# Kernel tuning notes

Hardware: AMD Instinct MI355X
Metric: run time of the kernel (lower is better)

The kernel has to match this reference:

```python
import jax, jax.numpy as jnp
import numpy as np

D_MODEL = 96
D_STATE = 16
D_INNER = 192   # expand * d_model
DT_RANK = 6     # ceil(96/16)
D_DEPTH_OUT = 1024  # (64/2)*(64/2)
BATCH, HH, WW = 2, 64, 64


def silu(v):
    return v * jax.nn.sigmoid(v)


def setup_inputs() -> dict:
    key = jax.random.key(0)
    ks = jax.random.split(key, 10)
    f = jnp.float32
    x = jax.random.normal(ks[0], (BATCH, HH, WW, D_MODEL), f)
    in_proj_w = jax.random.normal(ks[1], (2 * D_INNER, D_MODEL), f) * 0.02
    conv2d_w = jax.random.normal(ks[2], (D_INNER, 1, 3, 3), f) * 0.1  # depthwise, groups=D_INNER
    conv2d_b = jnp.zeros((D_INNER,), f)
    depth_conv_w = jax.random.normal(ks[3], (D_INNER, 1, 3, 3), f) * 0.1  # depthwise, stride 2
    depth_conv_b = jnp.zeros((D_INNER,), f)
    depth_fc_w = jax.random.normal(ks[4], (D_INNER, D_DEPTH_OUT), f) * 0.02
    depth_fc_b = jnp.zeros((D_INNER,), f)
    x_proj_w = jax.random.normal(ks[5], (DT_RANK + 2 * D_STATE, D_INNER), f) * 0.02
    dt_init_std = DT_RANK ** (-0.5)
    dt_projs_w = jax.random.uniform(ks[6], (D_INNER, DT_RANK), f, -dt_init_std, dt_init_std)
    # inverse-softplus of dt ~ U(log 1e-3, log 0.1)
    dt = jnp.exp(jax.random.uniform(ks[7], (D_INNER,), f) * (np.log(0.1) - np.log(0.001)) + np.log(0.001))
    dt = jnp.clip(dt, 1e-4, None)
    dt_projs_b = dt + jnp.log(-jnp.expm1(-dt))
    A_logs = jnp.log(jnp.tile(jnp.arange(1, D_STATE + 1, dtype=f)[None, :], (D_INNER, 1)))
    Ds = jnp.ones((D_INNER,), f)
    out_norm_w = jnp.ones((D_INNER,), f)
    out_norm_b = jnp.zeros((D_INNER,), f)
    out_proj_w = jax.random.normal(ks[8], (D_MODEL, D_INNER), f) * 0.02
    return dict(x=x, in_proj_w=in_proj_w, conv2d_w=conv2d_w, conv2d_b=conv2d_b,
                depth_conv_w=depth_conv_w, depth_conv_b=depth_conv_b,
                depth_fc_w=depth_fc_w, depth_fc_b=depth_fc_b, x_proj_w=x_proj_w,
                dt_projs_w=dt_projs_w, dt_projs_b=dt_projs_b, A_logs=A_logs, Ds=Ds,
                out_norm_w=out_norm_w, out_norm_b=out_norm_b, out_proj_w=out_proj_w)


def _selective_scan(u, delta, A, Bm, Cm, D, delta_bias):
    # u, delta: [B, D, L]; A: [D, N]; Bm, Cm: [B, N, L]; D: [D]; delta_bias: [D]
    delta = jax.nn.softplus(delta + delta_bias[None, :, None])
    dA = jnp.exp(jnp.einsum('bdl,dn->lbdn', delta, A))          # [L,B,D,N]
    dBu = jnp.einsum('bdl,bnl,bdl->lbdn', delta, Bm, u)          # [L,B,D,N]
    Ct = jnp.transpose(Cm, (2, 0, 1))                            # [L,B,N]
    h0 = jnp.zeros(dA.shape[1:], u.dtype)

    def step(h, inp):
        a, b, c = inp
        h = a * h + b                                            # S6 recurrence
        return h, jnp.einsum('bdn,bn->bd', h, c)

    _, ys = jax.lax.scan(step, h0, (dA, dBu, Ct))                # ys: [L,B,D]
    y = jnp.transpose(ys, (1, 2, 0))                             # [B,D,L]
    return y + D[None, :, None] * u


def _forward(x, in_proj_w, conv2d_w, conv2d_b, depth_conv_w, depth_conv_b,
             depth_fc_w, depth_fc_b, x_proj_w, dt_projs_w, dt_projs_b,
             A_logs, Ds, out_norm_w, out_norm_b, out_proj_w):
    B, H, W, _ = x.shape
    Di, N, R = D_INNER, D_STATE, DT_RANK
    dn = ('NCHW', 'OIHW', 'NCHW')
    xz = x @ in_proj_w.T
    x1, z = jnp.split(xz, 2, axis=-1)
    xc = jnp.transpose(x1, (0, 3, 1, 2))                         # [B,Di,H,W]
    xc = jax.lax.conv_general_dilated(xc, conv2d_w, (1, 1), [(1, 1), (1, 1)],
                                      dimension_numbers=dn, feature_group_count=Di)
    xc = silu(xc + conv2d_b[None, :, None, None])
    dxc = jax.lax.conv_general_dilated(xc, depth_conv_w, (2, 2), [(1, 1), (1, 1)],
                                       dimension_numbers=dn, feature_group_count=Di)
    dxc = dxc + depth_conv_b[None, :, None, None]                # [B,Di,H/2,W/2]
    dx = dxc.reshape(B, Di, -1)                                  # [B,Di,1024]
    dx = dx @ depth_fc_w.T + depth_fc_b                          # [B,Di,Di]
    dx = silu(jnp.transpose(dx, (0, 2, 1)))                      # [B,Di,CC], CC=Di
    L = H * W
    CC = dx.shape[-1]
    xs = jnp.concatenate([dx, xc.reshape(B, Di, L)], axis=-1)    # mode='head': [B,Di,LL]
    x_dbl = jnp.einsum('bdl,cd->bcl', xs, x_proj_w)
    dts, Bm, Cm = x_dbl[:, :R], x_dbl[:, R:R + N], x_dbl[:, R + N:]
    dts = jnp.einsum('brl,dr->bdl', dts, dt_projs_w)
    A = -jnp.exp(A_logs)
    y = _selective_scan(xs, dts, A, Bm, Cm, Ds, dt_projs_b)
    y = y[..., CC:]                                              # drop depth tokens (head mode)
    y = jnp.transpose(y, (0, 2, 1)).reshape(B, H, W, Di)
    mu = jnp.mean(y, axis=-1, keepdims=True)
    var = jnp.var(y, axis=-1, keepdims=True)
    y = (y - mu) * jax.lax.rsqrt(var + 1e-5) * out_norm_w + out_norm_b
    y = y * silu(z)
    return y @ out_proj_w.T


def reference(x, in_proj_w, conv2d_w, conv2d_b, depth_conv_w, depth_conv_b,
              depth_fc_w, depth_fc_b, x_proj_w, dt_projs_w, dt_projs_b,
              A_logs, Ds, out_norm_w, out_norm_b, out_proj_w):
    return _forward(x, in_proj_w, conv2d_w, conv2d_b, depth_conv_w, depth_conv_b,
                    depth_fc_w, depth_fc_b, x_proj_w, dt_projs_w, dt_projs_b,
                    A_logs, Ds, out_norm_w, out_norm_b, out_proj_w)
```

## Files before the change

kernel.cpp:

```cpp
#include <hip/hip_runtime.h>
#include <hip/hip_bf16.h>

typedef __hip_bfloat16 bf16;

#define BATCH 2
#define DM 96
#define DI 192
#define LSP 4096
#define LD 192
#define LTOT 4288
#define NST 16
#define RK 6
#define DFC 1024
#define CLEN 64
#define NCH 67
#define XR 16

__device__ __forceinline__ float b2f(bf16 v) { return __bfloat162float(v); }
__device__ __forceinline__ float silu_f(float x) { return x / (1.f + __expf(-x)); }
__device__ __forceinline__ float softplus_f(float x) { return x > 20.f ? x : log1pf(__expf(x)); }

__device__ __forceinline__ int is_f32(const void* alog) {
    return ((const unsigned int*)alog)[0] == 0u;
}
__device__ __forceinline__ float LDI(const void* p, int i, int f32m) {
    return f32m ? ((const float*)p)[i] : __bfloat162float(((const bf16*)p)[i]);
}
__device__ __forceinline__ void unpack2(unsigned int u, float* o) {
    o[0] = __uint_as_float(u << 16);
    o[1] = __uint_as_float(u & 0xffff0000u);
}

__global__ __launch_bounds__(256) void k_prep(const void* __restrict__ fw, const void* __restrict__ alog,
                                              float* __restrict__ Wt) {
    __shared__ float tile[64][65];
    const int f32m = is_f32(alog);
    int t = threadIdx.x;
    int kt = blockIdx.x & 15, jt = blockIdx.x >> 4;
    int k0 = kt * 64, j0 = jt * 64;
    int kk = t & 63, jj = t >> 6;
    for (int j = jj; j < 64; j += 4)
        tile[j][kk] = LDI(fw, (j0 + j) * DFC + k0 + kk, f32m);
    __syncthreads();
    for (int k = jj; k < 64; k += 4)
        Wt[(k0 + k) * DI + j0 + kk] = tile[kk][k];
}

__global__ __launch_bounds__(768) void k_inproj(const void* __restrict__ x, const void* __restrict__ ipw,
                                                const void* __restrict__ alog,
                                                float* __restrict__ x1, float* __restrict__ z) {
    __shared__ uint4 sxr[384];
    const int f32m = is_f32(alog);
    int t = threadIdx.x;
    int col = t >> 1;
    int kh = t & 1;
    int row0 = blockIdx.x * 16;
    float wr[48];
    if (f32m) {
        const float4* wp = (const float4*)((const float*)ipw + col * 96 + kh * 48);
        #pragma unroll
        for (int i = 0; i < 12; i++) {
            float4 v = wp[i];
            wr[4*i] = v.x; wr[4*i+1] = v.y; wr[4*i+2] = v.z; wr[4*i+3] = v.w;
        }
        if (t < 384) sxr[t] = ((const uint4*)((const float*)x + row0 * 96))[t];
        __syncthreads();
        for (int r = 0; r < 16; r++) {
            const uint4* xr = &sxr[r * 24 + kh * 12];
            float acc = 0.f;
            #pragma unroll
            for (int i = 0; i < 12; i++) {
                uint4 u = xr[i];
                acc += __uint_as_float(u.x) * wr[4*i]   + __uint_as_float(u.y) * wr[4*i+1]
                     + __uint_as_float(u.z) * wr[4*i+2] + __uint_as_float(u.w) * wr[4*i+3];
            }
            acc += __shfl_xor(acc, 1);
            if (kh == 0) {
                int row = row0 + r;
                if (col < DI) x1[row * DI + col] = acc;
                else          z[row * DI + (col - DI)] = acc;
            }
        }
    } else {
        const uint4* wp = (const uint4*)((const bf16*)ipw + col * 96 + kh * 48);
        #pragma unroll
        for (int i = 0; i < 6; i++) {
            uint4 v = wp[i];
            unpack2(v.x, &wr[8*i]);   unpack2(v.y, &wr[8*i+2]);
            unpack2(v.z, &wr[8*i+4]); unpack2(v.w, &wr[8*i+6]);
        }
        if (t < 192) sxr[t] = ((const uint4*)((const bf16*)x + row0 * 96))[t];
        __syncthreads();
        for (int r = 0; r < 16; r++) {
            const uint4* xr = &sxr[r * 12 + kh * 6];
            float acc = 0.f;
            #pragma unroll
            for (int i = 0; i < 6; i++) {
                uint4 xv = xr[i];
                float xf8[8];
                unpack2(xv.x, &xf8[0]); unpack2(xv.y, &xf8[2]);
                unpack2(xv.z, &xf8[4]); unpack2(xv.w, &xf8[6]);
                #pragma unroll
                for (int j = 0; j < 8; j++) acc += xf8[j] * wr[8*i + j];
            }
            acc += __shfl_xor(acc, 1);
            if (kh == 0) {
                int row = row0 + r;
                if (col < DI) x1[row * DI + col] = acc;
                else          z[row * DI + (col - DI)] = acc;
            }
        }
    }
}

__global__ __launch_bounds__(192) void k_conv1(const float* __restrict__ x1, const void* __restrict__ cw,
                                               const void* __restrict__ cb, float* __restrict__ xs,
                                               const void* __restrict__ alog) {
    const int f32m = is_f32(alog);
    int d = threadIdx.x;
    int blk = blockIdx.x;
    int b = blk >> 12, l = blk & 4095;
    int h = l >> 6, w_ = l & 63;
    float acc = LDI(cb, d, f32m);
    #pragma unroll
    for (int dh = 0; dh < 3; dh++) {
        int hh = h + dh - 1;
        if ((unsigned)hh >= 64u) continue;
        #pragma unroll
        for (int dw = 0; dw < 3; dw++) {
            int ww = w_ + dw - 1;
            if ((unsigned)ww >= 64u) continue;
            acc += x1[((b << 12) + (hh << 6) + ww) * DI + d] * LDI(cw, d * 9 + dh * 3 + dw, f32m);
        }
    }
    xs[(b * LTOT + LD + l) * DI + d] = silu_f(acc);
}

__global__ __launch_bounds__(192) void k_conv2(const float* __restrict__ xs, const void* __restrict__ dw,
                                               const void* __restrict__ db, float* __restrict__ dxc,
                                               const void* __restrict__ alog) {
    const int f32m = is_f32(alog);
    int d = threadIdx.x;
    int blk = blockIdx.x;
    int b = blk >> 10, lp = blk & 1023;
    int hp = lp >> 5, wp = lp & 31;
    float acc = LDI(db, d, f32m);
    #pragma unroll
    for (int dh = 0; dh < 3; dh++) {
        int h = 2 * hp + dh - 1;
        if ((unsigned)h >= 64u) continue;
        #pragma unroll
        for (int dw_ = 0; dw_ < 3; dw_++) {
            int w_ = 2 * wp + dw_ - 1;
            if ((unsigned)w_ >= 64u) continue;
            acc += xs[(b * LTOT + LD + (h << 6) + w_) * DI + d] * LDI(dw, d * 9 + dh * 3 + dw_, f32m);
        }
    }
    dxc[(b * DFC + lp) * DI + d] = acc;
}

__global__ __launch_bounds__(192) void k_dfc(const float* __restrict__ dxc, const float* __restrict__ Wt,
                                             float* __restrict__ part) {
    __shared__ float sdx[256 * 4];
    int t = threadIdx.x;
    int blk = blockIdx.x;
    int p = blk / 96;
    int rem = blk - p * 96;
    int b  = rem / 48;
    int i0 = (rem % 48) * 4;
    int k0 = p * 256;
    for (int idx = t; idx < 256 * 4; idx += 192) {
        int k = idx >> 2, pp = idx & 3;
        sdx[idx] = dxc[(b * DFC + k0 + k) * DI + i0 + pp];
    }
    __syncthreads();
    float a0 = 0.f, a1 = 0.f, a2 = 0.f, a3 = 0.f;
    #pragma unroll 8
    for (int k = 0; k < 256; k++) {
        float wv = Wt[(k0 + k) * DI + t];
        float4 sv = *(const float4*)&sdx[k * 4];
        a0 += sv.x * wv; a1 += sv.y * wv; a2 += sv.z * wv; a3 += sv.w * wv;
    }
    int ob = ((p * 2 + b) * 192 + i0) * DI + t;
    part[ob]          = a0;
    part[ob + DI]     = a1;
    part[ob + 2 * DI] = a2;
    part[ob + 3 * DI] = a3;
}

__global__ __launch_bounds__(256) void k_dfcc(const float* __restrict__ part, const void* __restrict__ fb,
                                              float* __restrict__ xs, const void* __restrict__ alog) {
    const int f32m = is_f32(alog);
    int g = blockIdx.x * 256 + threadIdx.x;
    int ch = g % DI;
    int tok = (g / DI) % 192;
    int b = g / (DI * 192);
    int stride = 2 * 192 * DI;
    int o = (b * 192 + tok) * DI + ch;
    float v = part[o] + part[o + stride] + part[o + 2 * stride] + part[o + 3 * stride];
    v += LDI(fb, ch, f32m);
    xs[(b * LTOT + tok) * DI + ch] = silu_f(v);
}

__global__ __launch_bounds__(256) void k_xdbl(const float* __restrict__ xs, const void* __restrict__ xpw,
                                              const void* __restrict__ dtw, const void* __restrict__ dtb,
                                              float* __restrict__ BCb, float* __restrict__ del,
                                              const void* __restrict__ alog) {
    __shared__ float sw[38 * 193];
    __shared__ float srow[XR][193];
    __shared__ float sdtw[DI * RK];
    __shared__ float sdtb[DI];
    __shared__ float sxd6[XR][8];
    const int f32m = is_f32(alog);
    int t = threadIdx.x;
    for (int c = t >> 3; c < 38; c += 32) {
        int seg = (t & 7) * 24;
        for (int k = seg; k < seg + 24; k++) sw[c * 193 + k] = LDI(xpw, c * DI + k, f32m);
    }
    for (int idx = t; idx < DI * RK; idx += 256) sdtw[idx] = LDI(dtw, idx, f32m);
    if (t < DI) sdtb[t] = LDI(dtb, t, f32m);
    int row0 = blockIdx.x * XR;
    for (int idx = t; idx < XR * DI; idx += 256) {
        int row = idx / DI, k = idx - row * DI;
        srow[row][k] = xs[(row0 + row) * DI + k];
    }
    __syncthreads();
    int r = t & 15, cg = t >> 4;
    float a0 = 0.f, a1 = 0.f, a2 = 0.f;
    const float* w0 = &sw[cg * 193];
    const float* w1 = &sw[(cg + 16) * 193];
    const float* w2 = (cg < 6) ? &sw[(cg + 32) * 193] : &sw[cg * 193];
    const float* xr = srow[r];
    #pragma unroll 8
    for (int k = 0; k < DI; k++) {
        float xv = xr[k];
        a0 += xv * w0[k];
        a1 += xv * w1[k];
        a2 += xv * w2[k];
    }
    int grow = row0 + r;
    if (cg < 6) sxd6[r][cg] = a0;
    else        BCb[grow * 32 + (cg - 6)] = a0;
    BCb[grow * 32 + (cg + 10)] = a1;
    if (cg < 6) BCb[grow * 32 + (cg + 26)] = a2;
    __syncthreads();
    float xd0 = sxd6[r][0], xd1 = sxd6[r][1], xd2 = sxd6[r][2];
    float xd3 = sxd6[r][3], xd4 = sxd6[r][4], xd5 = sxd6[r][5];
    #pragma unroll
    for (int dd = 0; dd < 12; dd++) {
        int d = cg * 12 + dd;
        const float* wv = &sdtw[d * RK];
        float dtv = sdtb[d] + xd0 * wv[0] + xd1 * wv[1] + xd2 * wv[2]
                            + xd3 * wv[3] + xd4 * wv[4] + xd5 * wv[5];
        srow[r][d] = softplus_f(dtv);
    }
    __syncthreads();
    for (int idx = t; idx < XR * DI; idx += 256) {
        int row = idx / DI, k = idx - row * DI;
        del[(row0 + row) * DI + k] = srow[row][k];
    }
}

__global__ __launch_bounds__(256) void k_scan1(const float* __restrict__ del, const float* __restrict__ xs,
                                               const float* __restrict__ BCb, const void* __restrict__ alog,
                                               float* __restrict__ Af, float* __restrict__ hf) {
    __shared__ float sdel[CLEN * 16];
    __shared__ float su[CLEN * 16];
    __shared__ float sbc[CLEN * 32];
    const int f32m = is_f32(alog);
    int t = threadIdx.x;
    int beta = blockIdx.x;
    int b = beta / (12 * NCH);
    int rem = beta - b * (12 * NCH);
    int dblk = rem / NCH, ch = rem - dblk * NCH;
    int d0 = dblk * 16, l0 = ch * CLEN;
    int bL = b * LTOT;
    for (int idx = t; idx < CLEN * 16; idx += 256) {
        int i = idx >> 4, dd = idx & 15;
        sdel[idx] = del[(bL + l0 + i) * DI + d0 + dd];
        su[idx]   = xs [(bL + l0 + i) * DI + d0 + dd];
    }
    for (int idx = t; idx < CLEN * 32; idx += 256) {
        int i = idx >> 5, c = idx & 31;
        sbc[idx] = BCb[(bL + l0 + i) * 32 + c];
    }
    __syncthreads();
    int dloc = t >> 4, n = t & 15;
    int d = d0 + dloc;
    float A = -__expf(LDI(alog, d * NST + n, f32m));
    float h = 0.f, ap = 1.f;
    #pragma unroll 4
    for (int i = 0; i < CLEN; i++) {
        float dt = sdel[(i << 4) | dloc];
        float u  = su[(i << 4) | dloc];
        float Bv = sbc[(i << 5) | n];
        float a = __expf(dt * A);
        h = a * h + dt * Bv * u;
        ap *= a;
    }
    int o = ((b * DI + d) * NCH + ch) * NST + n;
    Af[o] = ap;
    hf[o] = h;
}

__global__ __launch_bounds__(256) void k_scan2(const float* __restrict__ Af, const float* __restrict__ hf,
                                               float* __restrict__ He) {
    int t = threadIdx.x;
    int g = blockIdx.x * 16 + (t >> 4);
    int n = t & 15;
    int base = g * NCH * NST + n;
    float h = 0.f;
    for (int ch = 0; ch < NCH; ch++) {
        int o = base + ch * NST;
        He[o] = h;
        h = Af[o] * h + hf[o];
    }
}

__global__ __launch_bounds__(256) void k_scan3(const float* __restrict__ del, const float* __restrict__ xs,
                                               const float* __restrict__ BCb, const void* __restrict__ alog,
                                               const void* __restrict__ Dsv, const float* __restrict__ He,
                                               float* __restrict__ y) {
    __shared__ float sdel[CLEN * 16];
    __shared__ float su[CLEN * 16];
    __shared__ float sbc[CLEN * 32];
    const int f32m = is_f32(alog);
    int t = threadIdx.x;
    int beta = blockIdx.x;
    int b = beta / (12 * NCH);
    int rem = beta - b * (12 * NCH);
    int dblk = rem / NCH, ch = rem - dblk * NCH;
    int d0 = dblk * 16, l0 = ch * CLEN;
    int bL = b * LTOT;
    for (int idx = t; idx < CLEN * 16; idx += 256) {
        int i = idx >> 4, dd = idx & 15;
        sdel[idx] = del[(bL + l0 + i) * DI + d0 + dd];
        su[idx]   = xs [(bL + l0 + i) * DI + d0 + dd];
    }
    for (int idx = t; idx < CLEN * 32; idx += 256) {
        int i = idx >> 5, c = idx & 31;
        sbc[idx] = BCb[(bL + l0 + i) * 32 + c];
    }
    __syncthreads();
    int dloc = t >> 4, n = t & 15;
    int d = d0 + dloc;
    float A = -__expf(LDI(alog, d * NST + n, f32m));
    float Dv = LDI(Dsv, d, f32m);
    float h = He[((b * DI + d) * NCH + ch) * NST + n];
    for (int i = 0; i < CLEN; i++) {
        float dt = sdel[(i << 4) | dloc];
        float u  = su[(i << 4) | dloc];
        float Bv = sbc[(i << 5) | n];
        float Cv = sbc[(i << 5) | 16 | n];
        float a = __expf(dt * A);
        h = a * h + dt * Bv * u;
        float yv = h * Cv;
        #pragma unroll
        for (int m = 8; m; m >>= 1) yv += __shfl_xor(yv, m, 16);
        int l = l0 + i;
        if (n == 0 && l >= LD) y[(b * LSP + (l - LD)) * DI + d] = yv + Dv * u;
    }
}

__global__ __launch_bounds__(384) void k_out(const float* __restrict__ y, const float* __restrict__ z,
                                             const void* __restrict__ nw, const void* __restrict__ nb,
                                             const void* __restrict__ opw, void* __restrict__ out,
                                             const void* __restrict__ alog) {
    __shared__ float sg[2][DI];
    __shared__ float sred[2][2][3];
    const int f32m = is_f32(alog);
    int t = threadIdx.x;
    int m = t >> 2, kh = t & 3;
    float wr[48];
    if (f32m) {
        const float4* wp = (const float4*)((const float*)opw + m * DI + kh * 48);
        #pragma unroll
        for (int i = 0; i < 12; i++) {
            float4 v = wp[i];
            wr[4*i] = v.x; wr[4*i+1] = v.y; wr[4*i+2] = v.z; wr[4*i+3] = v.w;
        }
    } else {
        const uint4* wp = (const uint4*)((const bf16*)opw + m * DI + kh * 48);
        #pragma unroll
        for (int i = 0; i < 6; i++) {
            uint4 v = wp[i];
            unpack2(v.x, &wr[8*i]);   unpack2(v.y, &wr[8*i+2]);
            unpack2(v.z, &wr[8*i+4]); unpack2(v.w, &wr[8*i+6]);
        }
    }
    float nwv = 0.f, nbv = 0.f;
    if (t < DI) { nwv = LDI(nw, t, f32m); nbv = LDI(nb, t, f32m); }
    int wv_ = t >> 6;
    int row0 = blockIdx.x * 16;
    for (int pr = 0; pr < 8; pr++) {
        int r0 = row0 + pr * 2, r1 = r0 + 1;
        float y0 = 0.f, z0 = 0.f, y1 = 0.f, z1 = 0.f;
        if (t < DI) {
            y0 = y[r0 * DI + t]; z0 = z[r0 * DI + t];
            y1 = y[r1 * DI + t]; z1 = z[r1 * DI + t];
            float s0 = y0, q0 = y0 * y0, s1 = y1, q1 = y1 * y1;
            #pragma unroll
            for (int off = 32; off; off >>= 1) {
                s0 += __shfl_xor(s0, off); q0 += __shfl_xor(q0, off);
                s1 += __shfl_xor(s1, off); q1 += __shfl_xor(q1, off);
            }
            if ((t & 63) == 0) {
                sred[0][0][wv_] = s0; sred[0][1][wv_] = q0;
                sred[1][0][wv_] = s1; sred[1][1][wv_] = q1;
            }
        }
        __syncthreads();
        if (t < DI) {
            float S0  = sred[0][0][0] + sred[0][0][1] + sred[0][0][2];
            float Q0  = sred[0][1][0] + sred[0][1][1] + sred[0][1][2];
            float S1  = sred[1][0][0] + sred[1][0][1] + sred[1][0][2];
            float Q1  = sred[1][1][0] + sred[1][1][1] + sred[1][1][2];
            float mu0 = S0 * (1.f / 192.f), var0 = Q0 * (1.f / 192.f) - mu0 * mu0;
            float mu1 = S1 * (1.f / 192.f), var1 = Q1 * (1.f / 192.f) - mu1 * mu1;
            float g0 = (y0 - mu0) * rsqrtf(var0 + 1e-5f) * nwv + nbv;
            g0 *= z0 / (1.f + __expf(-z0));
            float g1 = (y1 - mu1) * rsqrtf(var1 + 1e-5f) * nwv + nbv;
            g1 *= z1 / (1.f + __expf(-z1));
            sg[0][t] = g0;
            sg[1][t] = g1;
        }
        __syncthreads();
        const float* g0p = &sg[0][kh * 48];
        const float* g1p = &sg[1][kh * 48];
        float a0 = 0.f, a1 = 0.f;
        #pragma unroll
        for (int j = 0; j < 48; j++) {
            a0 += g0p[j] * wr[j];
            a1 += g1p[j] * wr[j];
        }
        a0 += __shfl_xor(a0, 1); a0 += __shfl_xor(a0, 2);
        a1 += __shfl_xor(a1, 1); a1 += __shfl_xor(a1, 2);
        if (kh == 0) {
            if (f32m) {
                ((float*)out)[r0 * DM + m] = a0;
                ((float*)out)[r1 * DM + m] = a1;
            } else {
                ((bf16*)out)[r0 * DM + m] = __float2bfloat16(a0);
                ((bf16*)out)[r1 * DM + m] = __float2bfloat16(a1);
            }
        }
    }
}

extern "C" void kernel_launch(void* const* d_in, const int* in_sizes, int n_in,
                              void* d_out, int out_size, void* d_ws, size_t ws_size,
                              hipStream_t stream) {
    (void)in_sizes; (void)n_in; (void)out_size; (void)ws_size;
    const void* x    = d_in[0];
    const void* ipw  = d_in[1];
    const void* c1w  = d_in[2];
    const void* c1b  = d_in[3];
    const void* c2w  = d_in[4];
    const void* c2b  = d_in[5];
    const void* fcw  = d_in[6];
    const void* fcb  = d_in[7];
    const void* xpw  = d_in[8];
    const void* dtw  = d_in[9];
    const void* dtb  = d_in[10];
    const void* alog = d_in[11];
    const void* Dsv  = d_in[12];
    const void* nw   = d_in[13];
    const void* nb   = d_in[14];
    const void* opw  = d_in[15];

    float* ws  = (float*)d_ws;
    float* x1  = ws;
    float* z   = x1  + BATCH * LSP * DI;
    float* xs  = z   + BATCH * LSP * DI;
    float* dxc = xs  + BATCH * LTOT * DI;
    float* BCb = dxc + BATCH * DFC * DI;
    float* del = BCb + BATCH * LTOT * 32;
    float* Af  = del + BATCH * LTOT * DI;
    float* hf  = Af  + BATCH * DI * NCH * NST;
    float* He  = hf  + BATCH * DI * NCH * NST;
    float* Wt  = He  + BATCH * DI * NCH * NST;
    float* part = x1;
    float* y    = x1;

    k_prep  <<<dim3(48), dim3(256), 0, stream>>>(fcw, alog, Wt);
    k_inproj<<<dim3(512), dim3(768), 0, stream>>>(x, ipw, alog, x1, z);
    k_conv1 <<<dim3(BATCH * LSP), dim3(DI), 0, stream>>>(x1, c1w, c1b, xs, alog);
    k_conv2 <<<dim3(BATCH * DFC), dim3(DI), 0, stream>>>(xs, c2w, c2b, dxc, alog);
    k_dfc   <<<dim3(384), dim3(DI), 0, stream>>>(dxc, Wt, part);
    k_dfcc  <<<dim3(288), dim3(256), 0, stream>>>(part, fcb, xs, alog);
    k_xdbl  <<<dim3(536), dim3(256), 0, stream>>>(xs, xpw, dtw, dtb, BCb, del, alog);
    k_scan1 <<<dim3(BATCH * 12 * NCH), dim3(256), 0, stream>>>(del, xs, BCb, alog, Af, hf);
    k_scan2 <<<dim3(24), dim3(256), 0, stream>>>(Af, hf, He);
    k_scan3 <<<dim3(BATCH * 12 * NCH), dim3(256), 0, stream>>>(del, xs, BCb, alog, Dsv, He, y);
    k_out   <<<dim3(512), dim3(384), 0, stream>>>(y, z, nw, nb, opw, d_out, alog);
}
```

Measured before the change: 257.6 us.

## Fuse three-pass chunked scan into one persistent kernel with grid barriers

Merges the three scan kernels into a single kernel. Blocks keep their chunk data in shared memory and meet at two atomic-counter grid barriers, one before the inter-chunk carry pass and one before the output pass. The depth-FC combine (reduce partials, add bias, SiLU) moves into the x_dbl row load. The FC weight transpose prep kernel is removed by staging the original weight rows in shared memory. This saves launches and reloads of del/xs/BC, but the barrier relies on all 1608 blocks being co-resident, which risks deadlock or stalls, and the carry pass runs on only 24 blocks while the rest spin.

```diff
diff --git a/kernel.cpp b/kernel.cpp
--- a/kernel.cpp
+++ b/kernel.cpp
@@ -15,6 +15,7 @@
 #define CLEN 64
 #define NCH 67
 #define XR 16
+#define SCANBLK (BATCH * 12 * NCH)
 
 __device__ __forceinline__ float b2f(bf16 v) { return __bfloat162float(v); }
 __device__ __forceinline__ float silu_f(float x) { return x / (1.f + __expf(-x)); }
@@ -29,21 +30,6 @@
 __device__ __forceinline__ void unpack2(unsigned int u, float* o) {
     o[0] = __uint_as_float(u << 16);
     o[1] = __uint_as_float(u & 0xffff0000u);
-}
-
-__global__ __launch_bounds__(256) void k_prep(const void* __restrict__ fw, const void* __restrict__ alog,
-                                              float* __restrict__ Wt) {
-    __shared__ float tile[64][65];
-    const int f32m = is_f32(alog);
-    int t = threadIdx.x;
-    int kt = blockIdx.x & 15, jt = blockIdx.x >> 4;
-    int k0 = kt * 64, j0 = jt * 64;
-    int kk = t & 63, jj = t >> 6;
-    for (int j = jj; j < 64; j += 4)
-        tile[j][kk] = LDI(fw, (j0 + j) * DFC + k0 + kk, f32m);
-    __syncthreads();
-    for (int k = jj; k < 64; k += 4)
-        Wt[(k0 + k) * DI + j0 + kk] = tile[kk][k];
 }
 
 __global__ __launch_bounds__(768) void k_inproj(const void* __restrict__ x, const void* __restrict__ ipw,
@@ -159,53 +145,39 @@
     dxc[(b * DFC + lp) * DI + d] = acc;
 }
 
-__global__ __launch_bounds__(192) void k_dfc(const float* __restrict__ dxc, const float* __restrict__ Wt,
-                                             float* __restrict__ part) {
-    __shared__ float sdx[256 * 4];
+__global__ __launch_bounds__(192) void k_dfc(const float* __restrict__ dxc, const void* __restrict__ fw,
+                                             float* __restrict__ part, const void* __restrict__ alog) {
+    __shared__ float sfw[4 * 256];
+    const int f32m = is_f32(alog);
     int t = threadIdx.x;
     int blk = blockIdx.x;
     int p = blk / 96;
     int rem = blk - p * 96;
-    int b  = rem / 48;
-    int i0 = (rem % 48) * 4;
-    int k0 = p * 256;
-    for (int idx = t; idx < 256 * 4; idx += 192) {
-        int k = idx >> 2, pp = idx & 3;
-        sdx[idx] = dxc[(b * DFC + k0 + k) * DI + i0 + pp];
-    }
+    int b   = rem / 48;
+    int ch0 = (rem % 48) * 4;
+    int k0  = p * 256;
+    for (int idx = t; idx < 4 * 256; idx += 192)
+        sfw[idx] = LDI(fw, (ch0 + (idx >> 8)) * DFC + k0 + (idx & 255), f32m);
     __syncthreads();
     float a0 = 0.f, a1 = 0.f, a2 = 0.f, a3 = 0.f;
     #pragma unroll 8
     for (int k = 0; k < 256; k++) {
-        float wv = Wt[(k0 + k) * DI + t];
-        float4 sv = *(const float4*)&sdx[k * 4];
-        a0 += sv.x * wv; a1 += sv.y * wv; a2 += sv.z * wv; a3 += sv.w * wv;
-    }
-    int ob = ((p * 2 + b) * 192 + i0) * DI + t;
-    part[ob]          = a0;
-    part[ob + DI]     = a1;
-    part[ob + 2 * DI] = a2;
-    part[ob + 3 * DI] = a3;
-}
-
-__global__ __launch_bounds__(256) void k_dfcc(const float* __restrict__ part, const void* __restrict__ fb,
-                                              float* __restrict__ xs, const void* __restrict__ alog) {
-    const int f32m = is_f32(alog);
-    int g = blockIdx.x * 256 + threadIdx.x;
-    int ch = g % DI;
-    int tok = (g / DI) % 192;
-    int b = g / (DI * 192);
-    int stride = 2 * 192 * DI;
-    int o = (b * 192 + tok) * DI + ch;
-    float v = part[o] + part[o + stride] + part[o + 2 * stride] + part[o + 3 * stride];
-    v += LDI(fb, ch, f32m);
-    xs[(b * LTOT + tok) * DI + ch] = silu_f(v);
-}
-
-__global__ __launch_bounds__(256) void k_xdbl(const float* __restrict__ xs, const void* __restrict__ xpw,
+        float dv = dxc[(b * DFC + k0 + k) * DI + t];
+        a0 += dv * sfw[k];
+        a1 += dv * sfw[256 + k];
+        a2 += dv * sfw[512 + k];
+        a3 += dv * sfw[768 + k];
+    }
+    int ob = ((p * 2 + b) * 192 + t) * DI + ch0;
+    *(float4*)&part[ob] = make_float4(a0, a1, a2, a3);
+}
+
+__global__ __launch_bounds__(256) void k_xdbl(const float* __restrict__ xs_r, float* __restrict__ xs_w,
+                                              const float* __restrict__ part, const void* __restrict__ fb,
+                                              const void* __restrict__ xpw,
                                               const void* __restrict__ dtw, const void* __restrict__ dtb,
                                               float* __restrict__ BCb, float* __restrict__ del,
-                                              const void* __restrict__ alog) {
+                                              const void* __restrict__ alog, int* __restrict__ cnt) {
     __shared__ float sw[38 * 193];
     __shared__ float srow[XR][193];
     __shared__ float sdtw[DI * RK];
@@ -213,6 +185,7 @@
     __shared__ float sxd6[XR][8];
     const int f32m = is_f32(alog);
     int t = threadIdx.x;
+    if (blockIdx.x == 0 && t < 2) cnt[t] = 0;
     for (int c = t >> 3; c < 38; c += 32) {
         int seg = (t & 7) * 24;
         for (int k = seg; k < seg + 24; k++) sw[c * 193 + k] = LDI(xpw, c * DI + k, f32m);
@@ -220,9 +193,22 @@
     for (int idx = t; idx < DI * RK; idx += 256) sdtw[idx] = LDI(dtw, idx, f32m);
     if (t < DI) sdtb[t] = LDI(dtb, t, f32m);
     int row0 = blockIdx.x * XR;
+    int bb = row0 >= LTOT ? 1 : 0;
+    int depth = (row0 - bb * LTOT) < LD;
     for (int idx = t; idx < XR * DI; idx += 256) {
         int row = idx / DI, k = idx - row * DI;
-        srow[row][k] = xs[(row0 + row) * DI + k];
+        int grow = row0 + row;
+        float v;
+        if (depth) {
+            int tok = grow - bb * LTOT;
+            int o = (bb * 192 + tok) * DI + k;
+            v = part[o] + part[o + 73728] + part[o + 147456] + part[o + 221184];
+            v = silu_f(v + LDI(fb, k, f32m));
+            xs_w[grow * DI + k] = v;
+        } else {
+            v = xs_r[grow * DI + k];
+        }
+        srow[row][k] = v;
     }
     __syncthreads();
     int r = t & 15, cg = t >> 4;
@@ -261,9 +247,12 @@
     }
 }
 
-__global__ __launch_bounds__(256) void k_scan1(const float* __restrict__ del, const float* __restrict__ xs,
+__global__ __launch_bounds__(256) void k_scanF(const float* __restrict__ del, const float* __restrict__ xs,
                                                const float* __restrict__ BCb, const void* __restrict__ alog,
-                                               float* __restrict__ Af, float* __restrict__ hf) {
+                                               const void* __restrict__ Dsv,
+                                               float* __restrict__ Af, float* __restrict__ hf,
+                                               float* __restrict__ He, float* __restrict__ y,
+                                               int* __restrict__ cnt) {
     __shared__ float sdel[CLEN * 16];
     __shared__ float su[CLEN * 16];
     __shared__ float sbc[CLEN * 32];
@@ -288,6 +277,7 @@
     int dloc = t >> 4, n = t & 15;
     int d = d0 + dloc;
     float A = -__expf(LDI(alog, d * NST + n, f32m));
+    float Dv = LDI(Dsv, d, f32m);
     float h = 0.f, ap = 1.f;
     #pragma unroll 4
     for (int i = 0; i < CLEN; i++) {
@@ -301,52 +291,35 @@
     int o = ((b * DI + d) * NCH + ch) * NST + n;
     Af[o] = ap;
     hf[o] = h;
-}
-
-__global__ __launch_bounds__(256) void k_scan2(const float* __restrict__ Af, const float* __restrict__ hf,
-                                               float* __restrict__ He) {
-    int t = threadIdx.x;
-    int g = blockIdx.x * 16 + (t >> 4);
-    int n = t & 15;
-    int base = g * NCH * NST + n;
-    float h = 0.f;
-    for (int ch = 0; ch < NCH; ch++) {
-        int o = base + ch * NST;
-        He[o] = h;
-        h = Af[o] * h + hf[o];
-    }
-}
-
-__global__ __launch_bounds__(256) void k_scan3(const float* __restrict__ del, const float* __restrict__ xs,
-                                               const float* __restrict__ BCb, const void* __restrict__ alog,
-                                               const void* __restrict__ Dsv, const float* __restrict__ He,
-                                               float* __restrict__ y) {
-    __shared__ float sdel[CLEN * 16];
-    __shared__ float su[CLEN * 16];
-    __shared__ float sbc[CLEN * 32];
-    const int f32m = is_f32(alog);
-    int t = threadIdx.x;
-    int beta = blockIdx.x;
-    int b = beta / (12 * NCH);
-    int rem = beta - b * (12 * NCH);
-    int dblk = rem / NCH, ch = rem - dblk * NCH;
-    int d0 = dblk * 16, l0 = ch * CLEN;
-    int bL = b * LTOT;
-    for (int idx = t; idx < CLEN * 16; idx += 256) {
-        int i = idx >> 4, dd = idx & 15;
-        sdel[idx] = del[(bL + l0 + i) * DI + d0 + dd];
-        su[idx]   = xs [(bL + l0 + i) * DI + d0 + dd];
-    }
-    for (int idx = t; idx < CLEN * 32; idx += 256) {
-        int i = idx >> 5, c = idx & 31;
-        sbc[idx] = BCb[(bL + l0 + i) * 32 + c];
-    }
-    __syncthreads();
-    int dloc = t >> 4, n = t & 15;
-    int d = d0 + dloc;
-    float A = -__expf(LDI(alog, d * NST + n, f32m));
-    float Dv = LDI(Dsv, d, f32m);
-    float h = He[((b * DI + d) * NCH + ch) * NST + n];
+    __threadfence();
+    __syncthreads();
+    if (t == 0) {
+        atomicAdd(&cnt[0], 1);
+        while (__hip_atomic_load(&cnt[0], __ATOMIC_RELAXED, __HIP_MEMORY_SCOPE_AGENT) < SCANBLK)
+            __builtin_amdgcn_s_sleep(8);
+    }
+    __syncthreads();
+    __threadfence();
+    if (beta < 24) {
+        int g = beta * 16 + (t >> 4);
+        int base = g * NCH * NST + n;
+        float hh = 0.f;
+        for (int c2 = 0; c2 < NCH; c2++) {
+            int oo = base + c2 * NST;
+            He[oo] = hh;
+            hh = Af[oo] * hh + hf[oo];
+        }
+    }
+    __threadfence();
+    __syncthreads();
+    if (t == 0) {
+        atomicAdd(&cnt[1], 1);
+        while (__hip_atomic_load(&cnt[1], __ATOMIC_RELAXED, __HIP_MEMORY_SCOPE_AGENT) < SCANBLK)
+            __builtin_amdgcn_s_sleep(8);
+    }
+    __syncthreads();
+    __threadfence();
+    h = He[o];
     for (int i = 0; i < CLEN; i++) {
         float dt = sdel[(i << 4) | dloc];
         float u  = su[(i << 4) | dloc];
@@ -478,19 +451,15 @@
     float* Af  = del + BATCH * LTOT * DI;
     float* hf  = Af  + BATCH * DI * NCH * NST;
     float* He  = hf  + BATCH * DI * NCH * NST;
-    float* Wt  = He  + BATCH * DI * NCH * NST;
+    int*   cnt = (int*)(He + BATCH * DI * NCH * NST);
     float* part = x1;
     float* y    = x1;
 
-    k_prep  <<<dim3(48), dim3(256), 0, stream>>>(fcw, alog, Wt);
     k_inproj<<<dim3(512), dim3(768), 0, stream>>>(x, ipw, alog, x1, z);
     k_conv1 <<<dim3(BATCH * LSP), dim3(DI), 0, stream>>>(x1, c1w, c1b, xs, alog);
     k_conv2 <<<dim3(BATCH * DFC), dim3(DI), 0, stream>>>(xs, c2w, c2b, dxc, alog);
-    k_dfc   <<<dim3(384), dim3(DI), 0, stream>>>(dxc, Wt, part);
-    k_dfcc  <<<dim3(288), dim3(256), 0, stream>>>(part, fcb, xs, alog);
-    k_xdbl  <<<dim3(536), dim3(256), 0, stream>>>(xs, xpw, dtw, dtb, BCb, del, alog);
-    k_scan1 <<<dim3(BATCH * 12 * NCH), dim3(256), 0, stream>>>(del, xs, BCb, alog, Af, hf);
-    k_scan2 <<<dim3(24), dim3(256), 0, stream>>>(Af, hf, He);
-    k_scan3 <<<dim3(BATCH * 12 * NCH), dim3(256), 0, stream>>>(del, xs, BCb, alog, Dsv, He, y);
+    k_dfc   <<<dim3(384), dim3(DI), 0, stream>>>(dxc, fcw, part, alog);
+    k_xdbl  <<<dim3(536), dim3(256), 0, stream>>>(xs, xs, part, fcb, xpw, dtw, dtb, BCb, del, alog, cnt);
+    k_scanF <<<dim3(SCANBLK), dim3(256), 0, stream>>>(del, xs, BCb, alog, Dsv, Af, hf, He, y, cnt);
     k_out   <<<dim3(512), dim3(384), 0, stream>>>(y, z, nw, nb, opw, d_out, alog);
 }
```

Measured after the change: 806.2 us. 3.13x slower.
